# Performance work log

Hardware: AMD Instinct MI355X
Metric: run time of the kernel (lower is better)

The kernel has to match this reference:

```python
import jax, jax.numpy as jnp
import numpy as np

B, D, H = 16384, 64, 256

def setup_inputs() -> dict:
    key = jax.random.key(0)
    ks = jax.random.split(key, 24)
    s = 0.05
    inp = {
        'x':   jax.random.normal(ks[0], (B, D), dtype=jnp.float32),
        # stacked per-feature MLPs (torch ModuleList of Linear(1,H)->ReLU->Linear(H,H)->ReLU->Linear(H,1))
        'W1':  jax.random.normal(ks[1], (D, H), dtype=jnp.float32) * s,      # in=1
        'b1':  jax.random.normal(ks[2], (D, H), dtype=jnp.float32) * s,
        'W2':  jax.random.normal(ks[3], (D, H, H), dtype=jnp.float32) * s,
        'b2':  jax.random.normal(ks[4], (D, H), dtype=jnp.float32) * s,
        'W3':  jax.random.normal(ks[5], (D, H), dtype=jnp.float32) * s,      # out=1
        'b3':  jax.random.normal(ks[6], (D,), dtype=jnp.float32) * s,
        # attention fusion
        'Wq':  jax.random.normal(ks[7], (H, D), dtype=jnp.float32) * s,
        'bq':  jax.random.normal(ks[8], (H,), dtype=jnp.float32) * s,
        'Wk':  jax.random.normal(ks[9], (H, D), dtype=jnp.float32) * s,
        'bk':  jax.random.normal(ks[10], (H,), dtype=jnp.float32) * s,
        'Ws':  jax.random.normal(ks[11], (D, H), dtype=jnp.float32) * s,
        'bs':  jax.random.normal(ks[12], (D,), dtype=jnp.float32) * s,
        # cross MLP: Linear(D,H)->ReLU->Linear(H,1)
        'Wc1': jax.random.normal(ks[13], (H, D), dtype=jnp.float32) * s,
        'bc1': jax.random.normal(ks[14], (H,), dtype=jnp.float32) * s,
        'Wc2': jax.random.normal(ks[15], (H,), dtype=jnp.float32) * s,
        'bc2': jax.random.normal(ks[16], (1,), dtype=jnp.float32) * s,
        # g_func: Linear(1,H)->ReLU->Linear(H,1)
        'Wg1': jax.random.normal(ks[17], (H,), dtype=jnp.float32) * s,
        'bg1': jax.random.normal(ks[18], (H,), dtype=jnp.float32) * s,
        'Wg2': jax.random.normal(ks[19], (H,), dtype=jnp.float32) * s,
        'bg2': jax.random.normal(ks[20], (1,), dtype=jnp.float32) * s,
    }
    return inp

def reference(x, W1, b1, W2, b2, W3, b3, Wq, bq, Wk, bk, Ws, bs,
              Wc1, bc1, Wc2, bc2, Wg1, bg1, Wg2, bg2):
    # per-feature 3-layer MLPs, vectorized over the feature axis d
    a1 = jax.nn.relu(x[:, :, None] * W1[None] + b1[None])           # [B, D, H]
    a2 = jax.nn.relu(jnp.einsum('bdh,dhk->bdk', a1, W2) + b2[None]) # [B, D, H]
    h_cat = jnp.einsum('bdh,dh->bd', a2, W3) + b3[None]             # [B, D]
    # tiny tanh-softmax attention fusion
    q = h_cat @ Wq.T + bq                                           # [B, H]
    k = h_cat @ Wk.T + bk                                           # [B, H]
    scores = jnp.tanh(q * k) @ Ws.T + bs                            # [B, D]
    wts = jax.nn.softmax(scores, axis=1)
    weighted = jnp.sum(h_cat * wts, axis=1, keepdims=True)          # [B, 1]
    cross = jax.nn.relu(h_cat @ Wc1.T + bc1) @ Wc2[:, None] + bc2   # [B, 1]
    comb = weighted + cross                                         # [B, 1]
    out = jax.nn.relu(comb * Wg1[None] + bg1[None]) @ Wg2[:, None] + bg2  # [B, 1]
    return out
```

## Files before the change

kernel.cpp:

```cpp
#include <hip/hip_runtime.h>
#include <stdint.h>

#define Bn 16384
#define Dn 64
#define Hn 256

typedef short bf16x8 __attribute__((ext_vector_type(8)));
typedef float f32x4 __attribute__((ext_vector_type(4)));

__global__ __launch_bounds__(256) void xpose(const float* __restrict__ x,
                                             float* __restrict__ xT) {
  __shared__ float tile[64][65];
  int t = threadIdx.x;
  int r0 = blockIdx.x * 64;
  int c = t & 63, rr = t >> 6;
  #pragma unroll
  for (int i = 0; i < 16; ++i)
    tile[rr + i * 4][c] = x[(size_t)(r0 + rr + i * 4) * Dn + c];
  __syncthreads();
  #pragma unroll
  for (int i = 0; i < 16; ++i)
    xT[(size_t)(rr + i * 4) * Bn + r0 + c] = tile[c][rr + i * 4];
}

__global__ __launch_bounds__(256) void prep_t(
    const float* __restrict__ Wq, const float* __restrict__ Wk,
    const float* __restrict__ Wc1, const float* __restrict__ Ws,
    float* __restrict__ WqT, float* __restrict__ WkT,
    float* __restrict__ Wc1T, float* __restrict__ WsT) {
  int t = blockIdx.x * 256 + threadIdx.x;
  int h = t >> 6, dd = t & 63;
  WqT[dd * 256 + h]  = Wq[h * 64 + dd];
  WkT[dd * 256 + h]  = Wk[h * 64 + dd];
  Wc1T[dd * 256 + h] = Wc1[h * 64 + dd];
  WsT[h * 64 + dd]   = Ws[dd * 256 + h];
}

__global__ __launch_bounds__(512, 2) void gemm_hcat(
    const float* __restrict__ xT, const float* __restrict__ W1,
    const float* __restrict__ b1, const float* __restrict__ W2,
    const float* __restrict__ b2, const float* __restrict__ W3,
    const float* __restrict__ b3, float* __restrict__ hcT) {
  __shared__ char As[2][32768];
  __shared__ float P[2][4][64];

  int bid = blockIdx.x;
  int j = bid >> 3;
  int d = (bid & 7) * 8 + (j & 7);
  int base = (j >> 3) * 2048;

  int tid = threadIdx.x;
  int lane = tid & 63;
  int w = tid >> 6;
  int wm = w >> 2, wn = w & 3;
  int l15 = lane & 15;
  int g = lane >> 4;
  int ko = w * 4 + g;

  const float* W1d = W1 + d * Hn;
  const float* b1d = b1 + d * Hn;
  const float* W2d = W2 + (size_t)d * Hn * Hn;
  const float* xTd = xT + (size_t)d * Bn + base;

  float4 w1a = *(const float4*)(W1d + ko * 8);
  float4 w1b = *(const float4*)(W1d + ko * 8 + 4);
  float4 b1a = *(const float4*)(b1d + ko * 8);
  float4 b1b = *(const float4*)(b1d + ko * 8 + 4);

  float4 bvf[4], wvf[4];
  #pragma unroll
  for (int nj = 0; nj < 4; ++nj) {
    int col = wn * 64 + nj * 16 + g * 4;
    bvf[nj] = *(const float4*)(b2 + d * Hn + col);
    wvf[nj] = *(const float4*)(W3 + d * Hn + col);
  }

  bf16x8 breg[32];
  #pragma unroll
  for (int s = 0; s < 8; ++s)
    #pragma unroll
    for (int nj = 0; nj < 4; ++nj) {
      const float* src = W2d + (size_t)(s * 32 + g * 8) * Hn + wn * 64 + nj * 16 + l15;
      float u0 = src[0],        u1 = src[Hn],       u2 = src[2 * Hn], u3 = src[3 * Hn];
      float u4 = src[4 * Hn],   u5 = src[5 * Hn],   u6 = src[6 * Hn], u7 = src[7 * Hn];
      union { uint4 u; bf16x8 v; } pk;
      asm("v_cvt_pk_bf16_f32 %0, %1, %2" : "=v"(pk.u.x) : "v"(u0), "v"(u1));
      asm("v_cvt_pk_bf16_f32 %0, %1, %2" : "=v"(pk.u.y) : "v"(u2), "v"(u3));
      asm("v_cvt_pk_bf16_f32 %0, %1, %2" : "=v"(pk.u.z) : "v"(u4), "v"(u5));
      asm("v_cvt_pk_bf16_f32 %0, %1, %2" : "=v"(pk.u.w) : "v"(u6), "v"(u7));
      breg[s * 4 + nj] = pk.v;
    }

  #define A1CHUNK(wb, gm, xv)                                                   \
    {                                                                           \
      float v0 = fmaxf(fmaf((xv), w1a.x, b1a.x), 0.f);                          \
      float v1 = fmaxf(fmaf((xv), w1a.y, b1a.y), 0.f);                          \
      float v2 = fmaxf(fmaf((xv), w1a.z, b1a.z), 0.f);                          \
      float v3 = fmaxf(fmaf((xv), w1a.w, b1a.w), 0.f);                          \
      float v4 = fmaxf(fmaf((xv), w1b.x, b1b.x), 0.f);                          \
      float v5 = fmaxf(fmaf((xv), w1b.y, b1b.y), 0.f);                          \
      float v6 = fmaxf(fmaf((xv), w1b.z, b1b.z), 0.f);                          \
      float v7 = fmaxf(fmaf((xv), w1b.w, b1b.w), 0.f);                          \
      uint4 pk;                                                                 \
      asm("v_cvt_pk_bf16_f32 %0, %1, %2" : "=v"(pk.x) : "v"(v0), "v"(v1));      \
      asm("v_cvt_pk_bf16_f32 %0, %1, %2" : "=v"(pk.y) : "v"(v2), "v"(v3));      \
      asm("v_cvt_pk_bf16_f32 %0, %1, %2" : "=v"(pk.z) : "v"(v4), "v"(v5));      \
      asm("v_cvt_pk_bf16_f32 %0, %1, %2" : "=v"(pk.w) : "v"(v6), "v"(v7));      \
      *(uint4*)((wb) + (w * 4 + (gm)) * 1024 + lane * 16) = pk;                 \
    }

  {
    #pragma unroll
    for (int gm = 0; gm < 4; ++gm) {
      float xv = xTd[gm * 16 + l15];
      A1CHUNK(As[0], gm, xv);
    }
  }
  __syncthreads();

  float b3d = b3[d];
  for (int t = 0; t < 32; ++t) {
    int p = t & 1;
    const char* rb = As[p];
    char* wb = As[p ^ 1];
    bool pre = (t < 31);
    float xn[4];
    if (pre) {
      #pragma unroll
      for (int gm = 0; gm < 4; ++gm) xn[gm] = xTd[(t + 1) * 64 + gm * 16 + l15];
    }

    f32x4 acc[2][4];
    #pragma unroll
    for (int mi = 0; mi < 2; ++mi)
      #pragma unroll
      for (int nj = 0; nj < 4; ++nj) {
        f32x4 iv = {bvf[nj].x, bvf[nj].y, bvf[nj].z, bvf[nj].w};
        acc[mi][nj] = iv;
      }

    #pragma unroll
    for (int s = 0; s < 8; ++s) {
      bf16x8 af0 = *(const bf16x8*)(rb + (s * 4 + wm * 2) * 1024 + lane * 16);
      bf16x8 af1 = *(const bf16x8*)(rb + (s * 4 + wm * 2 + 1) * 1024 + lane * 16);
      if (pre && s < 4) { A1CHUNK(wb, s, xn[s]); }
      __builtin_amdgcn_s_setprio(1);
      #pragma unroll
      for (int nj = 0; nj < 4; ++nj) {
        acc[0][nj] = __builtin_amdgcn_mfma_f32_16x16x32_bf16(breg[s * 4 + nj], af0, acc[0][nj], 0, 0, 0);
        acc[1][nj] = __builtin_amdgcn_mfma_f32_16x16x32_bf16(breg[s * 4 + nj], af1, acc[1][nj], 0, 0, 0);
      }
      __builtin_amdgcn_s_setprio(0);
    }

    float* Pb = (float*)P[p];
    #pragma unroll
    for (int mi = 0; mi < 2; ++mi) {
      float ph = 0.f;
      #pragma unroll
      for (int nj = 0; nj < 4; ++nj) {
        ph = fmaf(fmaxf(acc[mi][nj][0], 0.f), wvf[nj].x, ph);
        ph = fmaf(fmaxf(acc[mi][nj][1], 0.f), wvf[nj].y, ph);
        ph = fmaf(fmaxf(acc[mi][nj][2], 0.f), wvf[nj].z, ph);
        ph = fmaf(fmaxf(acc[mi][nj][3], 0.f), wvf[nj].w, ph);
      }
      ph += __shfl_xor(ph, 16);
      ph += __shfl_xor(ph, 32);
      if (lane < 16) Pb[wn * 64 + wm * 32 + mi * 16 + l15] = ph;
    }
    __syncthreads();
    if (tid < 64)
      hcT[(size_t)d * Bn + base + t * 64 + tid] =
          Pb[tid] + Pb[64 + tid] + Pb[128 + tid] + Pb[192 + tid] + b3d;
  }
  #undef A1CHUNK
}

__global__ __launch_bounds__(256) void fused_tail(
    const float* __restrict__ hcT, const float* __restrict__ WqT,
    const float* __restrict__ bq, const float* __restrict__ WkT,
    const float* __restrict__ bk, const float* __restrict__ WsT,
    const float* __restrict__ bs, const float* __restrict__ Wc1T,
    const float* __restrict__ bc1, const float* __restrict__ Wc2,
    const float* __restrict__ bc2, const float* __restrict__ Wg1,
    const float* __restrict__ bg1, const float* __restrict__ Wg2,
    const float* __restrict__ bg2, float* __restrict__ out) {
  __shared__ float hcs[4][4][64];
  __shared__ float ts[4][4][256];
  int wid = threadIdx.x >> 6;
  int lane = threadIdx.x & 63;
  int r0 = (blockIdx.x * 4 + wid) * 4;
  float4 hc4 = *(const float4*)(hcT + (size_t)lane * Bn + r0);
  hcs[wid][0][lane] = hc4.x;
  hcs[wid][1][lane] = hc4.y;
  hcs[wid][2][lane] = hc4.z;
  hcs[wid][3][lane] = hc4.w;
  __syncthreads();

  float qv[4][4], kv[4][4], cv[4][4];
  #pragma unroll
  for (int j = 0; j < 4; ++j) {
    int h = lane + 64 * j;
    float bqv = bq[h], bkv = bk[h], bcv = bc1[h];
    #pragma unroll
    for (int r = 0; r < 4; ++r) { qv[r][j] = bqv; kv[r][j] = bkv; cv[r][j] = bcv; }
  }
  for (int d2 = 0; d2 < 64; ++d2) {
    float hv0 = hcs[wid][0][d2], hv1 = hcs[wid][1][d2];
    float hv2 = hcs[wid][2][d2], hv3 = hcs[wid][3][d2];
    #pragma unroll
    for (int j = 0; j < 4; ++j) {
      int h = lane + 64 * j;
      float wq = WqT[d2 * 256 + h], wk = WkT[d2 * 256 + h], wc = Wc1T[d2 * 256 + h];
      qv[0][j] = fmaf(wq, hv0, qv[0][j]); qv[1][j] = fmaf(wq, hv1, qv[1][j]);
      qv[2][j] = fmaf(wq, hv2, qv[2][j]); qv[3][j] = fmaf(wq, hv3, qv[3][j]);
      kv[0][j] = fmaf(wk, hv0, kv[0][j]); kv[1][j] = fmaf(wk, hv1, kv[1][j]);
      kv[2][j] = fmaf(wk, hv2, kv[2][j]); kv[3][j] = fmaf(wk, hv3, kv[3][j]);
      cv[0][j] = fmaf(wc, hv0, cv[0][j]); cv[1][j] = fmaf(wc, hv1, cv[1][j]);
      cv[2][j] = fmaf(wc, hv2, cv[2][j]); cv[3][j] = fmaf(wc, hv3, cv[3][j]);
    }
  }
  #pragma unroll
  for (int r = 0; r < 4; ++r)
    #pragma unroll
    for (int j = 0; j < 4; ++j)
      ts[wid][r][lane + 64 * j] = tanhf(qv[r][j] * kv[r][j]);
  __syncthreads();

  float sc[4];
  { float b = bs[lane]; sc[0] = b; sc[1] = b; sc[2] = b; sc[3] = b; }
  for (int h2 = 0; h2 < 256; ++h2) {
    float w = WsT[h2 * 64 + lane];
    sc[0] = fmaf(w, ts[wid][0][h2], sc[0]);
    sc[1] = fmaf(w, ts[wid][1][h2], sc[1]);
    sc[2] = fmaf(w, ts[wid][2][h2], sc[2]);
    sc[3] = fmaf(w, ts[wid][3][h2], sc[3]);
  }

  float hcr[4] = {hc4.x, hc4.y, hc4.z, hc4.w};
  float res[4];
  #pragma unroll
  for (int r = 0; r < 4; ++r) {
    float s = sc[r];
    float mx = s;
    #pragma unroll
    for (int off = 1; off < 64; off <<= 1) mx = fmaxf(mx, __shfl_xor(mx, off));
    float e = __expf(s - mx);
    float se = e;
    #pragma unroll
    for (int off = 1; off < 64; off <<= 1) se += __shfl_xor(se, off);
    float wgt = hcr[r] * (e / se);
    #pragma unroll
    for (int off = 1; off < 64; off <<= 1) wgt += __shfl_xor(wgt, off);
    float cp = 0.f;
    #pragma unroll
    for (int j = 0; j < 4; ++j) cp = fmaf(fmaxf(cv[r][j], 0.f), Wc2[lane + 64 * j], cp);
    #pragma unroll
    for (int off = 1; off < 64; off <<= 1) cp += __shfl_xor(cp, off);
    float comb = wgt + cp + bc2[0];
    float fp = 0.f;
    #pragma unroll
    for (int j = 0; j < 4; ++j) {
      int h = lane + 64 * j;
      fp = fmaf(fmaxf(fmaf(comb, Wg1[h], bg1[h]), 0.f), Wg2[h], fp);
    }
    #pragma unroll
    for (int off = 1; off < 64; off <<= 1) fp += __shfl_xor(fp, off);
    res[r] = fp + bg2[0];
  }
  if (lane == 0) {
    float4 o = make_float4(res[0], res[1], res[2], res[3]);
    *(float4*)(out + r0) = o;
  }
}

extern "C" void kernel_launch(void* const* d_in, const int* in_sizes, int n_in,
                              void* d_out, int out_size, void* d_ws, size_t ws_size,
                              hipStream_t stream) {
  const float* x   = (const float*)d_in[0];
  const float* W1  = (const float*)d_in[1];
  const float* b1  = (const float*)d_in[2];
  const float* W2  = (const float*)d_in[3];
  const float* b2  = (const float*)d_in[4];
  const float* W3  = (const float*)d_in[5];
  const float* b3  = (const float*)d_in[6];
  const float* Wq  = (const float*)d_in[7];
  const float* bq  = (const float*)d_in[8];
  const float* Wk  = (const float*)d_in[9];
  const float* bk  = (const float*)d_in[10];
  const float* Ws  = (const float*)d_in[11];
  const float* bs  = (const float*)d_in[12];
  const float* Wc1 = (const float*)d_in[13];
  const float* bc1 = (const float*)d_in[14];
  const float* Wc2 = (const float*)d_in[15];
  const float* bc2 = (const float*)d_in[16];
  const float* Wg1 = (const float*)d_in[17];
  const float* bg1 = (const float*)d_in[18];
  const float* Wg2 = (const float*)d_in[19];
  const float* bg2 = (const float*)d_in[20];

  float* hcT  = (float*)d_ws;
  float* xT   = (float*)((char*)d_ws + 4194304);
  float* WqT  = (float*)((char*)d_ws + 8388608);
  float* WkT  = WqT + 16384;
  float* Wc1T = WkT + 16384;
  float* WsT  = Wc1T + 16384;

  xpose<<<256, 256, 0, stream>>>(x, xT);
  prep_t<<<64, 256, 0, stream>>>(Wq, Wk, Wc1, Ws, WqT, WkT, Wc1T, WsT);
  gemm_hcat<<<512, 512, 0, stream>>>(xT, W1, b1, W2, b2, W3, b3, hcT);
  fused_tail<<<1024, 256, 0, stream>>>(hcT, WqT, bq, WkT, bk, WsT, bs, Wc1T, bc1,
                                       Wc2, bc2, Wg1, bg1, Wg2, bg2, (float*)d_out);
}
```

Baseline: 183.7 us.

## Split gemm_hcat output columns across two blocks and sum partials in tail

Result: slower. 392.2 us (+113.5%).

```diff
diff --git a/kernel.cpp b/kernel.cpp
--- a/kernel.cpp
+++ b/kernel.cpp
@@ -36,161 +36,172 @@
   WsT[h * 64 + dd]   = Ws[dd * 256 + h];
 }
 
-__global__ __launch_bounds__(512, 2) void gemm_hcat(
+__global__ __launch_bounds__(256, 4) void gemm_hcat(
     const float* __restrict__ xT, const float* __restrict__ W1,
     const float* __restrict__ b1, const float* __restrict__ W2,
     const float* __restrict__ b2, const float* __restrict__ W3,
-    const float* __restrict__ b3, float* __restrict__ hcT) {
-  __shared__ char As[2][32768];
-  __shared__ float P[2][4][64];
+    float* __restrict__ hcP) {
+  __shared__ char As[2][16384];
+  __shared__ float P[2][4][32];
 
   int bid = blockIdx.x;
-  int j = bid >> 3;
-  int d = (bid & 7) * 8 + (j & 7);
-  int base = (j >> 3) * 2048;
+  int xcd = bid & 7;
+  int rest = bid >> 3;
+  int dl = rest & 7;
+  int half = (rest >> 3) & 1;
+  int chunk = rest >> 4;
+  int d = xcd * 8 + dl;
+  int base = chunk * 1024;
 
   int tid = threadIdx.x;
   int lane = tid & 63;
   int w = tid >> 6;
-  int wm = w >> 2, wn = w & 3;
   int l15 = lane & 15;
   int g = lane >> 4;
-  int ko = w * 4 + g;
-
+  int colbase = half * 128 + w * 32;
+
+  const float* W2d = W2 + (size_t)d * Hn * Hn;
+  const float* xTd = xT + (size_t)d * Bn + base;
   const float* W1d = W1 + d * Hn;
   const float* b1d = b1 + d * Hn;
-  const float* W2d = W2 + (size_t)d * Hn * Hn;
-  const float* xTd = xT + (size_t)d * Bn + base;
-
-  float4 w1a = *(const float4*)(W1d + ko * 8);
-  float4 w1b = *(const float4*)(W1d + ko * 8 + 4);
-  float4 b1a = *(const float4*)(b1d + ko * 8);
-  float4 b1b = *(const float4*)(b1d + ko * 8 + 4);
-
-  float4 bvf[4], wvf[4];
-  #pragma unroll
-  for (int nj = 0; nj < 4; ++nj) {
-    int col = wn * 64 + nj * 16 + g * 4;
-    bvf[nj] = *(const float4*)(b2 + d * Hn + col);
-    wvf[nj] = *(const float4*)(W3 + d * Hn + col);
-  }
-
-  bf16x8 breg[32];
+  const float* b2d = b2 + d * Hn;
+  const float* W3d = W3 + d * Hn;
+
+  bf16x8 breg[16];
   #pragma unroll
   for (int s = 0; s < 8; ++s)
     #pragma unroll
-    for (int nj = 0; nj < 4; ++nj) {
-      const float* src = W2d + (size_t)(s * 32 + g * 8) * Hn + wn * 64 + nj * 16 + l15;
-      float u0 = src[0],        u1 = src[Hn],       u2 = src[2 * Hn], u3 = src[3 * Hn];
-      float u4 = src[4 * Hn],   u5 = src[5 * Hn],   u6 = src[6 * Hn], u7 = src[7 * Hn];
+    for (int nj = 0; nj < 2; ++nj) {
+      const float* src = W2d + (size_t)(s * 32 + g * 8) * Hn + colbase + nj * 16 + l15;
+      float u0 = src[0],      u1 = src[Hn],     u2 = src[2 * Hn], u3 = src[3 * Hn];
+      float u4 = src[4 * Hn], u5 = src[5 * Hn], u6 = src[6 * Hn], u7 = src[7 * Hn];
       union { uint4 u; bf16x8 v; } pk;
       asm("v_cvt_pk_bf16_f32 %0, %1, %2" : "=v"(pk.u.x) : "v"(u0), "v"(u1));
       asm("v_cvt_pk_bf16_f32 %0, %1, %2" : "=v"(pk.u.y) : "v"(u2), "v"(u3));
       asm("v_cvt_pk_bf16_f32 %0, %1, %2" : "=v"(pk.u.z) : "v"(u4), "v"(u5));
       asm("v_cvt_pk_bf16_f32 %0, %1, %2" : "=v"(pk.u.w) : "v"(u6), "v"(u7));
-      breg[s * 4 + nj] = pk.v;
-    }
-
-  #define A1CHUNK(wb, gm, xv)                                                   \
+      breg[s * 2 + nj] = pk.v;
+    }
+
+  #define A1CHUNK(wbuf, c, xv)                                                  \
     {                                                                           \
-      float v0 = fmaxf(fmaf((xv), w1a.x, b1a.x), 0.f);                          \
-      float v1 = fmaxf(fmaf((xv), w1a.y, b1a.y), 0.f);                          \
-      float v2 = fmaxf(fmaf((xv), w1a.z, b1a.z), 0.f);                          \
-      float v3 = fmaxf(fmaf((xv), w1a.w, b1a.w), 0.f);                          \
-      float v4 = fmaxf(fmaf((xv), w1b.x, b1b.x), 0.f);                          \
-      float v5 = fmaxf(fmaf((xv), w1b.y, b1b.y), 0.f);                          \
-      float v6 = fmaxf(fmaf((xv), w1b.z, b1b.z), 0.f);                          \
-      float v7 = fmaxf(fmaf((xv), w1b.w, b1b.w), 0.f);                          \
+      int st = 2 * w + ((c) & 1);                                               \
+      int k0 = st * 32 + g * 8;                                                 \
+      float4 wa = *(const float4*)(W1d + k0);                                   \
+      float4 wbq = *(const float4*)(W1d + k0 + 4);                              \
+      float4 ba = *(const float4*)(b1d + k0);                                   \
+      float4 bbq = *(const float4*)(b1d + k0 + 4);                              \
+      float v0 = fmaxf(fmaf((xv), wa.x, ba.x), 0.f);                            \
+      float v1 = fmaxf(fmaf((xv), wa.y, ba.y), 0.f);                            \
+      float v2 = fmaxf(fmaf((xv), wa.z, ba.z), 0.f);                            \
+      float v3 = fmaxf(fmaf((xv), wa.w, ba.w), 0.f);                            \
+      float v4 = fmaxf(fmaf((xv), wbq.x, bbq.x), 0.f);                          \
+      float v5 = fmaxf(fmaf((xv), wbq.y, bbq.y), 0.f);                          \
+      float v6 = fmaxf(fmaf((xv), wbq.z, bbq.z), 0.f);                          \
+      float v7 = fmaxf(fmaf((xv), wbq.w, bbq.w), 0.f);                          \
       uint4 pk;                                                                 \
       asm("v_cvt_pk_bf16_f32 %0, %1, %2" : "=v"(pk.x) : "v"(v0), "v"(v1));      \
       asm("v_cvt_pk_bf16_f32 %0, %1, %2" : "=v"(pk.y) : "v"(v2), "v"(v3));      \
       asm("v_cvt_pk_bf16_f32 %0, %1, %2" : "=v"(pk.z) : "v"(v4), "v"(v5));      \
       asm("v_cvt_pk_bf16_f32 %0, %1, %2" : "=v"(pk.w) : "v"(v6), "v"(v7));      \
-      *(uint4*)((wb) + (w * 4 + (gm)) * 1024 + lane * 16) = pk;                 \
+      *(uint4*)((wbuf) + (st * 2 + ((c) >> 1)) * 1024 + lane * 16) = pk;        \
     }
 
   {
-    #pragma unroll
-    for (int gm = 0; gm < 4; ++gm) {
-      float xv = xTd[gm * 16 + l15];
-      A1CHUNK(As[0], gm, xv);
-    }
+    float x0 = xTd[l15];
+    float x1 = xTd[16 + l15];
+    A1CHUNK(As[0], 0, x0);
+    A1CHUNK(As[0], 1, x0);
+    A1CHUNK(As[0], 2, x1);
+    A1CHUNK(As[0], 3, x1);
   }
   __syncthreads();
 
-  float b3d = b3[d];
+  float* hcPd = hcP + ((size_t)half * Dn + d) * Bn + base;
+
   for (int t = 0; t < 32; ++t) {
     int p = t & 1;
     const char* rb = As[p];
     char* wb = As[p ^ 1];
     bool pre = (t < 31);
-    float xn[4];
+    float xn[2];
     if (pre) {
+      xn[0] = xTd[(t + 1) * 32 + l15];
+      xn[1] = xTd[(t + 1) * 32 + 16 + l15];
+    }
+
+    f32x4 acc[2][2];
+    {
+      float4 bv0 = *(const float4*)(b2d + colbase + g * 4);
+      float4 bv1 = *(const float4*)(b2d + colbase + 16 + g * 4);
+      f32x4 i0 = {bv0.x, bv0.y, bv0.z, bv0.w};
+      f32x4 i1 = {bv1.x, bv1.y, bv1.z, bv1.w};
+      acc[0][0] = i0; acc[1][0] = i0;
+      acc[0][1] = i1; acc[1][1] = i1;
+    }
+
+    #pragma unroll
+    for (int s = 0; s < 8; ++s) {
+      bf16x8 af0 = *(const bf16x8*)(rb + (s * 2 + 0) * 1024 + lane * 16);
+      bf16x8 af1 = *(const bf16x8*)(rb + (s * 2 + 1) * 1024 + lane * 16);
+      if (pre && s < 4) { A1CHUNK(wb, s, xn[s >> 1]); }
+      __builtin_amdgcn_s_setprio(1);
+      acc[0][0] = __builtin_amdgcn_mfma_f32_16x16x32_bf16(breg[s * 2 + 0], af0, acc[0][0], 0, 0, 0);
+      acc[1][0] = __builtin_amdgcn_mfma_f32_16x16x32_bf16(breg[s * 2 + 0], af1, acc[1][0], 0, 0, 0);
+      acc[0][1] = __builtin_amdgcn_mfma_f32_16x16x32_bf16(breg[s * 2 + 1], af0, acc[0][1], 0, 0, 0);
+      acc[1][1] = __builtin_amdgcn_mfma_f32_16x16x32_bf16(breg[s * 2 + 1], af1, acc[1][1], 0, 0, 0);
+      __builtin_amdgcn_s_setprio(0);
+    }
+
+    {
+      float4 wv0 = *(const float4*)(W3d + colbase + g * 4);
+      float4 wv1 = *(const float4*)(W3d + colbase + 16 + g * 4);
+      float* Pb = (float*)P[p];
       #pragma unroll
-      for (int gm = 0; gm < 4; ++gm) xn[gm] = xTd[(t + 1) * 64 + gm * 16 + l15];
-    }
-
-    f32x4 acc[2][4];
-    #pragma unroll
-    for (int mi = 0; mi < 2; ++mi)
-      #pragma unroll
-      for (int nj = 0; nj < 4; ++nj) {
-        f32x4 iv = {bvf[nj].x, bvf[nj].y, bvf[nj].z, bvf[nj].w};
-        acc[mi][nj] = iv;
+      for (int mi = 0; mi < 2; ++mi) {
+        float ph;
+        ph = fmaxf(acc[mi][0][0], 0.f) * wv0.x;
+        ph = fmaf(fmaxf(acc[mi][0][1], 0.f), wv0.y, ph);
+        ph = fmaf(fmaxf(acc[mi][0][2], 0.f), wv0.z, ph);
+        ph = fmaf(fmaxf(acc[mi][0][3], 0.f), wv0.w, ph);
+        ph = fmaf(fmaxf(acc[mi][1][0], 0.f), wv1.x, ph);
+        ph = fmaf(fmaxf(acc[mi][1][1], 0.f), wv1.y, ph);
+        ph = fmaf(fmaxf(acc[mi][1][2], 0.f), wv1.z, ph);
+        ph = fmaf(fmaxf(acc[mi][1][3], 0.f), wv1.w, ph);
+        ph += __shfl_xor(ph, 16);
+        ph += __shfl_xor(ph, 32);
+        if (lane < 16) Pb[w * 32 + mi * 16 + l15] = ph;
       }
-
-    #pragma unroll
-    for (int s = 0; s < 8; ++s) {
-      bf16x8 af0 = *(const bf16x8*)(rb + (s * 4 + wm * 2) * 1024 + lane * 16);
-      bf16x8 af1 = *(const bf16x8*)(rb + (s * 4 + wm * 2 + 1) * 1024 + lane * 16);
-      if (pre && s < 4) { A1CHUNK(wb, s, xn[s]); }
-      __builtin_amdgcn_s_setprio(1);
-      #pragma unroll
-      for (int nj = 0; nj < 4; ++nj) {
-        acc[0][nj] = __builtin_amdgcn_mfma_f32_16x16x32_bf16(breg[s * 4 + nj], af0, acc[0][nj], 0, 0, 0);
-        acc[1][nj] = __builtin_amdgcn_mfma_f32_16x16x32_bf16(breg[s * 4 + nj], af1, acc[1][nj], 0, 0, 0);
-      }
-      __builtin_amdgcn_s_setprio(0);
-    }
-
-    float* Pb = (float*)P[p];
-    #pragma unroll
-    for (int mi = 0; mi < 2; ++mi) {
-      float ph = 0.f;
-      #pragma unroll
-      for (int nj = 0; nj < 4; ++nj) {
-        ph = fmaf(fmaxf(acc[mi][nj][0], 0.f), wvf[nj].x, ph);
-        ph = fmaf(fmaxf(acc[mi][nj][1], 0.f), wvf[nj].y, ph);
-        ph = fmaf(fmaxf(acc[mi][nj][2], 0.f), wvf[nj].z, ph);
-        ph = fmaf(fmaxf(acc[mi][nj][3], 0.f), wvf[nj].w, ph);
-      }
-      ph += __shfl_xor(ph, 16);
-      ph += __shfl_xor(ph, 32);
-      if (lane < 16) Pb[wn * 64 + wm * 32 + mi * 16 + l15] = ph;
     }
     __syncthreads();
-    if (tid < 64)
-      hcT[(size_t)d * Bn + base + t * 64 + tid] =
-          Pb[tid] + Pb[64 + tid] + Pb[128 + tid] + Pb[192 + tid] + b3d;
+    if (tid < 32) {
+      float* Pb = (float*)P[p];
+      hcPd[t * 32 + tid] = Pb[tid] + Pb[32 + tid] + Pb[64 + tid] + Pb[96 + tid];
+    }
   }
   #undef A1CHUNK
 }
 
 __global__ __launch_bounds__(256) void fused_tail(
-    const float* __restrict__ hcT, const float* __restrict__ WqT,
-    const float* __restrict__ bq, const float* __restrict__ WkT,
-    const float* __restrict__ bk, const float* __restrict__ WsT,
-    const float* __restrict__ bs, const float* __restrict__ Wc1T,
-    const float* __restrict__ bc1, const float* __restrict__ Wc2,
-    const float* __restrict__ bc2, const float* __restrict__ Wg1,
-    const float* __restrict__ bg1, const float* __restrict__ Wg2,
-    const float* __restrict__ bg2, float* __restrict__ out) {
+    const float* __restrict__ hcP, const float* __restrict__ b3,
+    const float* __restrict__ WqT, const float* __restrict__ bq,
+    const float* __restrict__ WkT, const float* __restrict__ bk,
+    const float* __restrict__ WsT, const float* __restrict__ bs,
+    const float* __restrict__ Wc1T, const float* __restrict__ bc1,
+    const float* __restrict__ Wc2, const float* __restrict__ bc2,
+    const float* __restrict__ Wg1, const float* __restrict__ bg1,
+    const float* __restrict__ Wg2, const float* __restrict__ bg2,
+    float* __restrict__ out) {
   __shared__ float hcs[4][4][64];
   __shared__ float ts[4][4][256];
   int wid = threadIdx.x >> 6;
   int lane = threadIdx.x & 63;
   int r0 = (blockIdx.x * 4 + wid) * 4;
-  float4 hc4 = *(const float4*)(hcT + (size_t)lane * Bn + r0);
+  float4 p0 = *(const float4*)(hcP + (size_t)lane * Bn + r0);
+  float4 p1 = *(const float4*)(hcP + ((size_t)Dn + lane) * Bn + r0);
+  float b3v = b3[lane];
+  float4 hc4 = make_float4(p0.x + p1.x + b3v, p0.y + p1.y + b3v,
+                           p0.z + p1.z + b3v, p0.w + p1.w + b3v);
   hcs[wid][0][lane] = hc4.x;
   hcs[wid][1][lane] = hc4.y;
   hcs[wid][2][lane] = hc4.z;
@@ -299,16 +310,16 @@
   const float* Wg2 = (const float*)d_in[19];
   const float* bg2 = (const float*)d_in[20];
 
-  float* hcT  = (float*)d_ws;
-  float* xT   = (float*)((char*)d_ws + 4194304);
-  float* WqT  = (float*)((char*)d_ws + 8388608);
+  float* hcP  = (float*)d_ws;
+  float* xT   = (float*)((char*)d_ws + 8388608);
+  float* WqT  = (float*)((char*)d_ws + 12582912);
   float* WkT  = WqT + 16384;
   float* Wc1T = WkT + 16384;
   float* WsT  = Wc1T + 16384;
 
   xpose<<<256, 256, 0, stream>>>(x, xT);
   prep_t<<<64, 256, 0, stream>>>(Wq, Wk, Wc1, Ws, WqT, WkT, Wc1T, WsT);
-  gemm_hcat<<<512, 512, 0, stream>>>(xT, W1, b1, W2, b2, W3, b3, hcT);
-  fused_tail<<<1024, 256, 0, stream>>>(hcT, WqT, bq, WkT, bk, WsT, bs, Wc1T, bc1,
+  gemm_hcat<<<2048, 256, 0, stream>>>(xT, W1, b1, W2, b2, W3, hcP);
+  fused_tail<<<1024, 256, 0, stream>>>(hcP, b3, WqT, bq, WkT, bk, WsT, bs, Wc1T, bc1,
                                        Wc2, bc2, Wg1, bg1, Wg2, bg2, (float*)d_out);
 }
```
